# Performance work log

Measured on AMD Instinct MI355X. Metric: run time of the kernel, lower is better.

## Reference

```python
import jax, jax.numpy as jnp
import numpy as np

BATCH = 16384
N_FEATURES = 768
FT_OUT = 1024
ACTIVE_P = 32.0 / 768.0  # ~32 active features per board, like real positions


def setup_inputs() -> dict:
    key = jax.random.key(0)
    k1, k2, k3, k4, k5, k6 = jax.random.split(key, 6)
    # densified sparse one-hot boards: binary {0,1} with ~32/768 density
    board_stm = (jax.random.uniform(k1, (BATCH, N_FEATURES)) < ACTIVE_P).astype(jnp.float32)
    board_nstm = (jax.random.uniform(k2, (BATCH, N_FEATURES)) < ACTIVE_P).astype(jnp.float32)
    # Linear(768, FT_OUT): weight [out, in], bias [out]
    W_ft = jax.random.normal(k3, (FT_OUT, N_FEATURES), dtype=jnp.float32) * (1.0 / np.sqrt(N_FEATURES))
    b_ft = jax.random.normal(k4, (FT_OUT,), dtype=jnp.float32) * 0.01
    # Linear(2*FT_OUT, 1)
    W_out = jax.random.normal(k5, (1, 2 * FT_OUT), dtype=jnp.float32) * (1.0 / np.sqrt(2 * FT_OUT))
    b_out = jax.random.normal(k6, (1,), dtype=jnp.float32) * 0.01
    return {"board_stm": board_stm, "board_nstm": board_nstm,
            "W_ft": W_ft, "b_ft": b_ft, "W_out": W_out, "b_out": b_out}


def screlu(x):
    # SCReLU: clamp(x, 0, 1)^2
    return jnp.square(jnp.clip(x, 0.0, 1.0))


def reference(board_stm, board_nstm, W_ft, b_ft, W_out, b_out):
    # feature transformer applied to both perspectives (shared weights)
    stm = jnp.einsum('bf,of->bo', board_stm, W_ft) + b_ft   # [B, FT_OUT]
    nstm = jnp.einsum('bf,of->bo', board_nstm, W_ft) + b_ft  # [B, FT_OUT]
    hidden = screlu(jnp.concatenate([stm, nstm], axis=1))    # [B, 2*FT_OUT]
    out = jnp.einsum('bh,oh->bo', hidden, W_out) + b_out     # [B, 1]
    return jax.nn.sigmoid(out)
```

## Files before the change

### kernel.cpp

```cpp
#include <hip/hip_runtime.h>
#include <stdint.h>

#define BATCH 16384
#define NF 768
#define FT 1024
#define RBB 32
#define GR 64
#define THREADS 256
#define NKS 12
#define ABLK (NKS * 4 * 64 * 16)

typedef int i32x4 __attribute__((ext_vector_type(4)));

__global__ __launch_bounds__(192) void prep_wq(const float* __restrict__ W_ft,
                                               char* __restrict__ Wq,
                                               float* __restrict__ invs) {
    const int o = blockIdx.x;
    const int t = threadIdx.x;
    __shared__ float smax[3];
    __shared__ float sscale;
    const float4 v = *(const float4*)(W_ft + (size_t)o * NF + t * 4);
    float m = fmaxf(fmaxf(fabsf(v.x), fabsf(v.y)), fmaxf(fabsf(v.z), fabsf(v.w)));
    #pragma unroll
    for (int s = 32; s > 0; s >>= 1) m = fmaxf(m, __shfl_down(m, s, 64));
    if ((t & 63) == 0) smax[t >> 6] = m;
    __syncthreads();
    if (t == 0) {
        const float am = fmaxf(fmaxf(smax[0], smax[1]), smax[2]);
        sscale = 127.0f / am;
        invs[o] = am / 127.0f;
    }
    __syncthreads();
    const float s = sscale;
    const float arr[4] = {v.x, v.y, v.z, v.w};
    uint32_t pk = 0;
    #pragma unroll
    for (int j = 0; j < 4; ++j) {
        const int q = (int)rintf(arr[j] * s);
        pk |= ((uint32_t)(unsigned char)(char)q) << (8 * j);
    }
    *(uint32_t*)(Wq + (size_t)o * NF + t * 4) = pk;
}

__device__ __forceinline__ uint32_t pack01(float4 v) {
    return (uint32_t)(v.x != 0.0f) | ((uint32_t)(v.y != 0.0f) << 8)
         | ((uint32_t)(v.z != 0.0f) << 16) | ((uint32_t)(v.w != 0.0f) << 24);
}

__global__ __launch_bounds__(THREADS, 2) void nnue_mfma(
    const float* __restrict__ bstm, const float* __restrict__ bnstm,
    const char* __restrict__ Wq, const float* __restrict__ invs,
    const float* __restrict__ b_ft, const float* __restrict__ W_out,
    const float* __restrict__ b_out, float* __restrict__ out)
{
    __shared__ __align__(16) char Albs[ABLK];
    __shared__ float red[GR][4];

    const int t = threadIdx.x;
    const int w = t >> 6;
    const int l = t & 63;
    const int b0 = blockIdx.x * RBB;

    #pragma unroll
    for (int bt = 0; bt < 3; ++bt) {
        float4 v[16];
        int rows[4], c16s[4];
        #pragma unroll
        for (int u = 0; u < 4; ++u) {
            const int chunkid = (bt * 4 + u) * THREADS + t;
            const int row = chunkid / 48;
            const int c16 = chunkid - row * 48;
            rows[u] = row; c16s[u] = c16;
            const float* src = ((row < RBB)
                ? (bstm + (size_t)(b0 + row) * NF)
                : (bnstm + (size_t)(b0 + row - RBB) * NF)) + c16 * 16;
            #pragma unroll
            for (int k = 0; k < 4; ++k)
                v[u * 4 + k] = *(const float4*)(src + k * 4);
        }
        __builtin_amdgcn_sched_barrier(0);
        #pragma unroll
        for (int u = 0; u < 4; ++u) {
            const int row = rows[u], c16 = c16s[u];
            const int r = row >> 4, cl2 = row & 15;
            const int ks = c16 >> 2, qq = c16 & 3;
            uint4 o;
            o.x = pack01(v[u * 4 + 0]); o.y = pack01(v[u * 4 + 1]);
            o.z = pack01(v[u * 4 + 2]); o.w = pack01(v[u * 4 + 3]);
            const int slot = ((ks * 4 + r) << 6) + (qq << 4) + cl2;
            *(uint4*)(&Albs[(size_t)slot << 4]) = o;
        }
    }
    __syncthreads();

    const int cl = l & 15;
    const int q = l >> 4;
    const i32x4* af = (const i32x4*)Albs;
    float ps[4][4] = {};

    #pragma unroll
    for (int ch = 0; ch < 4; ++ch) {
        const int colbase = ch * 256 + w * 64;
        const char* bp = Wq + (size_t)(colbase + cl) * NF + q * 16;

        i32x4 bcur[4];
        #pragma unroll
        for (int c = 0; c < 4; ++c)
            bcur[c] = *(const i32x4*)(bp + (size_t)c * 16 * NF);

        float iv[4], bf[4], wos[4], won[4];
        #pragma unroll
        for (int c = 0; c < 4; ++c) {
            const int col = colbase + c * 16 + cl;
            iv[c] = invs[col]; bf[c] = b_ft[col];
            wos[c] = W_out[col]; won[c] = W_out[FT + col];
        }

        i32x4 acc[4][4];
        #pragma unroll
        for (int r = 0; r < 4; ++r)
            #pragma unroll
            for (int c = 0; c < 4; ++c)
                acc[r][c] = (i32x4){0, 0, 0, 0};

        #pragma unroll
        for (int ks = 0; ks < NKS; ++ks) {
            i32x4 bnxt[4];
            if (ks < NKS - 1) {
                #pragma unroll
                for (int c = 0; c < 4; ++c)
                    bnxt[c] = *(const i32x4*)(bp + (size_t)c * 16 * NF + (ks + 1) * 64);
            }
            __builtin_amdgcn_s_setprio(1);
            #pragma unroll
            for (int r = 0; r < 4; ++r) {
                const i32x4 a = af[(ks * 4 + r) * 64 + l];
                #pragma unroll
                for (int c = 0; c < 4; ++c)
                    acc[r][c] = __builtin_amdgcn_mfma_i32_16x16x64_i8(
                        a, bcur[c], acc[r][c], 0, 0, 0);
            }
            __builtin_amdgcn_s_setprio(0);
            #pragma unroll
            for (int c = 0; c < 4; ++c) bcur[c] = bnxt[c];
        }

        #pragma unroll
        for (int c = 0; c < 4; ++c) {
            #pragma unroll
            for (int r = 0; r < 4; ++r) {
                const float wo = (r < 2) ? wos[c] : won[c];
                #pragma unroll
                for (int j = 0; j < 4; ++j) {
                    float h = fmaf((float)acc[r][c][j], iv[c], bf[c]);
                    h = fminf(fmaxf(h, 0.0f), 1.0f);
                    ps[r][j] = fmaf(h * h, wo, ps[r][j]);
                }
            }
        }
    }

    #pragma unroll
    for (int r = 0; r < 4; ++r)
        #pragma unroll
        for (int j = 0; j < 4; ++j) {
            float v = ps[r][j];
            v += __shfl_xor(v, 1, 64);
            v += __shfl_xor(v, 2, 64);
            v += __shfl_xor(v, 4, 64);
            v += __shfl_xor(v, 8, 64);
            if (cl == 0) red[16 * r + 4 * q + j][w] = v;
        }
    __syncthreads();

    if (t < RBB) {
        float x = b_out[0];
        #pragma unroll
        for (int w2 = 0; w2 < 4; ++w2)
            x += red[t][w2] + red[RBB + t][w2];
        out[b0 + t] = 1.0f / (1.0f + expf(-x));
    }
}

extern "C" void kernel_launch(void* const* d_in, const int* in_sizes, int n_in,
                              void* d_out, int out_size, void* d_ws, size_t ws_size,
                              hipStream_t stream) {
    const float* board_stm  = (const float*)d_in[0];
    const float* board_nstm = (const float*)d_in[1];
    const float* W_ft       = (const float*)d_in[2];
    const float* b_ft       = (const float*)d_in[3];
    const float* W_out      = (const float*)d_in[4];
    const float* b_out      = (const float*)d_in[5];
    float* out = (float*)d_out;

    char* Wq = (char*)d_ws;
    float* invs = (float*)((char*)d_ws + (size_t)FT * NF);

    prep_wq<<<FT, 192, 0, stream>>>(W_ft, Wq, invs);
    nnue_mfma<<<BATCH / RBB, THREADS, 0, stream>>>(
        board_stm, board_nstm, Wq, invs, b_ft, W_out, b_out, out);
}
```

Baseline: 89.33 us.

## Stage int8 weights through LDS with async global_load_lds triple buffering

Doubles the block to 8 waves, so each wave owns 128 output columns across two halves and keeps 32 accumulator tiles in registers instead of looping over 4 column chunks. Weight tiles are now streamed into a 3-slot LDS ring with global_load_lds and manual vmcnt waits, replacing per-lane register prefetch from global memory. The A-tile load is overlapped with issuing the first weight stages. Register pressure (128 accumulator registers) and the larger LDS footprint may reduce occupancy. The hand-written waitcnt sequencing is fragile.

```diff
diff --git a/kernel.cpp b/kernel.cpp
--- a/kernel.cpp
+++ b/kernel.cpp
@@ -6,9 +6,12 @@
 #define FT 1024
 #define RBB 32
 #define GR 64
-#define THREADS 256
+#define THREADS 512
 #define NKS 12
-#define ABLK (NKS * 4 * 64 * 16)
+#define NPH 24
+#define ABYTES (NKS * 4 * 64 * 16)
+#define BSLOT 4096
+#define BBYTES (3 * 8 * BSLOT)
 
 typedef int i32x4 __attribute__((ext_vector_type(4)));
 
@@ -47,119 +50,121 @@
          | ((uint32_t)(v.z != 0.0f) << 16) | ((uint32_t)(v.w != 0.0f) << 24);
 }
 
+__device__ __forceinline__ void gload16(const void* g, void* l) {
+    __builtin_amdgcn_global_load_lds(
+        (const __attribute__((address_space(1))) unsigned int*)g,
+        (__attribute__((address_space(3))) unsigned int*)l, 16, 0, 0);
+}
+
 __global__ __launch_bounds__(THREADS, 2) void nnue_mfma(
     const float* __restrict__ bstm, const float* __restrict__ bnstm,
     const char* __restrict__ Wq, const float* __restrict__ invs,
     const float* __restrict__ b_ft, const float* __restrict__ W_out,
     const float* __restrict__ b_out, float* __restrict__ out)
 {
-    __shared__ __align__(16) char Albs[ABLK];
-    __shared__ float red[GR][4];
+    __shared__ __align__(16) char Albs[ABYTES];
+    __shared__ __align__(16) char Bbs[BBYTES];
+    __shared__ float red[GR][8];
 
     const int t = threadIdx.x;
     const int w = t >> 6;
     const int l = t & 63;
-    const int b0 = blockIdx.x * RBB;
-
-    #pragma unroll
-    for (int bt = 0; bt < 3; ++bt) {
-        float4 v[16];
-        int rows[4], c16s[4];
-        #pragma unroll
-        for (int u = 0; u < 4; ++u) {
-            const int chunkid = (bt * 4 + u) * THREADS + t;
-            const int row = chunkid / 48;
-            const int c16 = chunkid - row * 48;
-            rows[u] = row; c16s[u] = c16;
-            const float* src = ((row < RBB)
-                ? (bstm + (size_t)(b0 + row) * NF)
-                : (bnstm + (size_t)(b0 + row - RBB) * NF)) + c16 * 16;
-            #pragma unroll
-            for (int k = 0; k < 4; ++k)
-                v[u * 4 + k] = *(const float4*)(src + k * 4);
-        }
-        __builtin_amdgcn_sched_barrier(0);
-        #pragma unroll
-        for (int u = 0; u < 4; ++u) {
-            const int row = rows[u], c16 = c16s[u];
-            const int r = row >> 4, cl2 = row & 15;
-            const int ks = c16 >> 2, qq = c16 & 3;
-            uint4 o;
-            o.x = pack01(v[u * 4 + 0]); o.y = pack01(v[u * 4 + 1]);
-            o.z = pack01(v[u * 4 + 2]); o.w = pack01(v[u * 4 + 3]);
-            const int slot = ((ks * 4 + r) << 6) + (qq << 4) + cl2;
-            *(uint4*)(&Albs[(size_t)slot << 4]) = o;
-        }
-    }
-    __syncthreads();
-
     const int cl = l & 15;
     const int q = l >> 4;
+    const int b0 = blockIdx.x * RBB;
+
+    #pragma unroll
+    for (int bt = 0; bt < 2; ++bt) {
+        float4 v[12];
+        int row[3], c16[3];
+        #pragma unroll
+        for (int j = 0; j < 3; ++j) {
+            const int id = (bt * 3 + j) * THREADS + t;
+            row[j] = id / 48; c16[j] = id - row[j] * 48;
+            const float* src = ((row[j] < RBB)
+                ? (bstm + (size_t)(b0 + row[j]) * NF)
+                : (bnstm + (size_t)(b0 + row[j] - RBB) * NF)) + c16[j] * 16;
+            #pragma unroll
+            for (int k = 0; k < 4; ++k)
+                v[j * 4 + k] = *(const float4*)(src + k * 4);
+        }
+        __builtin_amdgcn_sched_barrier(0);
+        #pragma unroll
+        for (int j = 0; j < 3; ++j) {
+            uint4 o;
+            o.x = pack01(v[j * 4 + 0]); o.y = pack01(v[j * 4 + 1]);
+            o.z = pack01(v[j * 4 + 2]); o.w = pack01(v[j * 4 + 3]);
+            const int ks = c16[j] >> 2, qq = c16[j] & 3;
+            const int rr = row[j] >> 4, c2 = row[j] & 15;
+            const int slotA = ((ks * 4 + rr) << 6) + (qq << 4) + c2;
+            *(uint4*)(&Albs[(size_t)slotA << 4]) = o;
+        }
+    }
+
+    const int srcLaneOff = cl * NF + q * 16;
+    auto issueB = [&](int p) {
+        const int slot = p % 3;
+        const int ks = p >> 1;
+        const int colbase = (p & 1) * 512 + w * 64;
+        #pragma unroll
+        for (int c = 0; c < 4; ++c)
+            gload16(Wq + (size_t)(colbase + c * 16) * NF + ks * 64 + srcLaneOff,
+                    Bbs + ((slot * 8 + w) * 4 + c) * 1024);
+    };
+    issueB(0); issueB(1); issueB(2);
+    __syncthreads();
+
     const i32x4* af = (const i32x4*)Albs;
+    i32x4 acc[4][8] = {};
+    i32x4 a[4];
+    #pragma unroll
+    for (int p = 0; p < NPH; ++p) {
+        const int slot = p % 3;
+        const int h = p & 1;
+        const int ks = p >> 1;
+        if (p < NPH - 2)       asm volatile("s_waitcnt vmcnt(8)" ::: "memory");
+        else if (p == NPH - 2) asm volatile("s_waitcnt vmcnt(4)" ::: "memory");
+        else                   asm volatile("s_waitcnt vmcnt(0)" ::: "memory");
+        i32x4 b[4];
+        #pragma unroll
+        for (int c = 0; c < 4; ++c)
+            b[c] = *(const i32x4*)(Bbs + ((slot * 8 + w) * 4 + c) * 1024 + l * 16);
+        if (h == 0) {
+            #pragma unroll
+            for (int r = 0; r < 4; ++r)
+                a[r] = af[(ks * 4 + r) * 64 + l];
+        }
+        asm volatile("s_waitcnt lgkmcnt(0)" ::: "memory");
+        if (p + 3 < NPH) issueB(p + 3);
+        __builtin_amdgcn_s_setprio(1);
+        #pragma unroll
+        for (int r = 0; r < 4; ++r)
+            #pragma unroll
+            for (int c = 0; c < 4; ++c)
+                acc[r][h * 4 + c] = __builtin_amdgcn_mfma_i32_16x16x64_i8(
+                    a[r], b[c], acc[r][h * 4 + c], 0, 0, 0);
+        __builtin_amdgcn_s_setprio(0);
+    }
+
     float ps[4][4] = {};
-
-    #pragma unroll
-    for (int ch = 0; ch < 4; ++ch) {
-        const int colbase = ch * 256 + w * 64;
-        const char* bp = Wq + (size_t)(colbase + cl) * NF + q * 16;
-
-        i32x4 bcur[4];
-        #pragma unroll
-        for (int c = 0; c < 4; ++c)
-            bcur[c] = *(const i32x4*)(bp + (size_t)c * 16 * NF);
-
-        float iv[4], bf[4], wos[4], won[4];
-        #pragma unroll
-        for (int c = 0; c < 4; ++c) {
-            const int col = colbase + c * 16 + cl;
-            iv[c] = invs[col]; bf[c] = b_ft[col];
-            wos[c] = W_out[col]; won[c] = W_out[FT + col];
-        }
-
-        i32x4 acc[4][4];
-        #pragma unroll
-        for (int r = 0; r < 4; ++r)
-            #pragma unroll
-            for (int c = 0; c < 4; ++c)
-                acc[r][c] = (i32x4){0, 0, 0, 0};
-
-        #pragma unroll
-        for (int ks = 0; ks < NKS; ++ks) {
-            i32x4 bnxt[4];
-            if (ks < NKS - 1) {
-                #pragma unroll
-                for (int c = 0; c < 4; ++c)
-                    bnxt[c] = *(const i32x4*)(bp + (size_t)c * 16 * NF + (ks + 1) * 64);
+    #pragma unroll
+    for (int cc = 0; cc < 8; ++cc) {
+        const int col = (cc >> 2) * 512 + w * 64 + (cc & 3) * 16 + cl;
+        const float iv = invs[col];
+        const float bf = b_ft[col];
+        const float wo0 = W_out[col];
+        const float wo1 = W_out[FT + col];
+        #pragma unroll
+        for (int r = 0; r < 4; ++r) {
+            const float wo = (r < 2) ? wo0 : wo1;
+            #pragma unroll
+            for (int j = 0; j < 4; ++j) {
+                float hh = fmaf((float)acc[r][cc][j], iv, bf);
+                hh = fminf(fmaxf(hh, 0.0f), 1.0f);
+                ps[r][j] = fmaf(hh * hh, wo, ps[r][j]);
             }
-            __builtin_amdgcn_s_setprio(1);
-            #pragma unroll
-            for (int r = 0; r < 4; ++r) {
-                const i32x4 a = af[(ks * 4 + r) * 64 + l];
-                #pragma unroll
-                for (int c = 0; c < 4; ++c)
-                    acc[r][c] = __builtin_amdgcn_mfma_i32_16x16x64_i8(
-                        a, bcur[c], acc[r][c], 0, 0, 0);
-            }
-            __builtin_amdgcn_s_setprio(0);
-            #pragma unroll
-            for (int c = 0; c < 4; ++c) bcur[c] = bnxt[c];
-        }
-
-        #pragma unroll
-        for (int c = 0; c < 4; ++c) {
-            #pragma unroll
-            for (int r = 0; r < 4; ++r) {
-                const float wo = (r < 2) ? wos[c] : won[c];
-                #pragma unroll
-                for (int j = 0; j < 4; ++j) {
-                    float h = fmaf((float)acc[r][c][j], iv[c], bf[c]);
-                    h = fminf(fmaxf(h, 0.0f), 1.0f);
-                    ps[r][j] = fmaf(h * h, wo, ps[r][j]);
-                }
-            }
-        }
-    }
-
+        }
+    }
     #pragma unroll
     for (int r = 0; r < 4; ++r)
         #pragma unroll
@@ -176,7 +181,7 @@
     if (t < RBB) {
         float x = b_out[0];
         #pragma unroll
-        for (int w2 = 0; w2 < 4; ++w2)
+        for (int w2 = 0; w2 < 8; ++w2)
             x += red[t][w2] + red[RBB + t][w2];
         out[b0 + t] = 1.0f / (1.0f + expf(-x));
     }
```

Measured after the change: 75.70 us. -15.3%, faster.
